# Optimization experiments

Measured on AMD Instinct MI355X. Metric: run time of the kernel, lower is better.

## Reference

```python
import jax, jax.numpy as jnp
import numpy as np

R, N, IN_F, OUT_F = 8, 4096, 64, 64


def setup_inputs() -> dict:
    key = jax.random.key(0)
    k_adj, k_x, k_w = jax.random.split(key, 3)
    adjacency = jax.random.uniform(k_adj, (R, N, N), dtype=jnp.float32)
    x = jax.random.normal(k_x, (N, IN_F), dtype=jnp.float32)
    weight = jax.random.uniform(k_w, (R, OUT_F, IN_F), dtype=jnp.float32)
    return {"adjacency": adjacency, "x": x, "weight": weight}


def reference(adjacency, x, weight):
    # y = sum_r (A[r] @ x) @ W[r].T
    # messages: [R, N, IN_F]
    msgs = jnp.einsum("rnm,mi->rni", adjacency, x)
    # transform per relation and sum over relations: [N, OUT_F]
    y = jnp.einsum("rni,roi->no", msgs, weight)
    return y
```

## Files before the change

kernel.cpp:

```cpp
#include <hip/hip_runtime.h>
#include <hip/hip_bf16.h>

#define RR 8
#define NN 4096
#define FF 64

typedef float f32x4 __attribute__((ext_vector_type(4)));
typedef short bf16x8 __attribute__((ext_vector_type(8)));

__device__ __forceinline__ short f2b(float f) {
  __hip_bfloat16 h = __float2bfloat16(f);
  return __builtin_bit_cast(short, h);
}

__device__ __forceinline__ bf16x8 cvt8(f32x4 lo, f32x4 hi) {
  bf16x8 r;
  r[0] = f2b(lo[0]); r[1] = f2b(lo[1]); r[2] = f2b(lo[2]); r[3] = f2b(lo[3]);
  r[4] = f2b(hi[0]); r[5] = f2b(hi[1]); r[6] = f2b(hi[2]); r[7] = f2b(hi[3]);
  return r;
}

__global__ __launch_bounds__(256) void compute_zt(const float* __restrict__ x,
                                                  const float* __restrict__ w,
                                                  short* __restrict__ zt) {
  const int tid   = threadIdx.x;
  const int lane  = tid & 63;
  const int wv    = tid >> 6;
  const int row16 = lane & 15;
  const int quad  = lane >> 4;
  const int r     = blockIdx.y;
  const int m0    = blockIdx.x * 64 + wv * 16;

  bf16x8 bfr[2];
#pragma unroll
  for (int s = 0; s < 2; ++s) {
    const float* p = x + (size_t)(m0 + row16) * FF + s * 32 + quad * 8;
    bfr[s] = cvt8(*(const f32x4*)p, *(const f32x4*)(p + 4));
  }

  f32x4 acc[4] = {{0.f,0.f,0.f,0.f},{0.f,0.f,0.f,0.f},
                  {0.f,0.f,0.f,0.f},{0.f,0.f,0.f,0.f}};
#pragma unroll
  for (int og = 0; og < 4; ++og) {
#pragma unroll
    for (int s = 0; s < 2; ++s) {
      const float* p = w + ((size_t)r * FF + og * 16 + row16) * FF + s * 32 + quad * 8;
      bf16x8 afr = cvt8(*(const f32x4*)p, *(const f32x4*)(p + 4));
      acc[og] = __builtin_amdgcn_mfma_f32_16x16x32_bf16(afr, bfr[s], acc[og], 0, 0, 0);
    }
  }

#pragma unroll
  for (int og = 0; og < 4; ++og)
#pragma unroll
    for (int j = 0; j < 4; ++j) {
      int o = og * 16 + quad * 4 + j;
      int m = m0 + row16;
      zt[((size_t)r * FF + o) * NN + m] = f2b(acc[og][j]);
    }
}


#define BK    128
#define NSTG  16
#define LROW  136

__device__ __forceinline__ void issueA(const float* __restrict__ abase,
                                       int trow, int tcol, int s, f32x4* av) {
#pragma unroll
  for (int i = 0; i < 8; ++i)
    av[i] = *(const f32x4*)(abase + (size_t)(i * 8 + trow) * NN + s * BK + tcol);
}

__device__ __forceinline__ void writeA(short* __restrict__ buf,
                                       int trow, int tcol, const f32x4* av) {
#pragma unroll
  for (int i = 0; i < 8; ++i) {
    short4 wv4;
    wv4.x = f2b(av[i][0]); wv4.y = f2b(av[i][1]);
    wv4.z = f2b(av[i][2]); wv4.w = f2b(av[i][3]);
    *(short4*)(buf + (i * 8 + trow) * LROW + tcol) = wv4;
  }
}

__device__ __forceinline__ void loadB4(const short* __restrict__ zb, int k, bf16x8* b) {
#pragma unroll
  for (int cg = 0; cg < 4; ++cg)
    b[cg] = *(const bf16x8*)(zb + (size_t)cg * 16 * NN + k);
}

__device__ __forceinline__ void mfma4(bf16x8 a, const bf16x8* b, f32x4* acc) {
  acc[0] = __builtin_amdgcn_mfma_f32_16x16x32_bf16(a, b[0], acc[0], 0, 0, 0);
  acc[1] = __builtin_amdgcn_mfma_f32_16x16x32_bf16(a, b[1], acc[1], 0, 0, 0);
  acc[2] = __builtin_amdgcn_mfma_f32_16x16x32_bf16(a, b[2], acc[2], 0, 0, 0);
  acc[3] = __builtin_amdgcn_mfma_f32_16x16x32_bf16(a, b[3], acc[3], 0, 0, 0);
}

__global__ __launch_bounds__(256, 3) void rgcn_main(const float* __restrict__ adj,
                                                    const short* __restrict__ zt,
                                                    float* __restrict__ partial) {
  __shared__ short lds[2][64 * LROW];

  const int tid   = threadIdx.x;
  const int lane  = tid & 63;
  const int wv    = tid >> 6;
  const int row16 = lane & 15;
  const int quad  = lane >> 4;

  const int nt   = blockIdx.x;
  const int rk   = blockIdx.y;
  const int r    = rk >> 1;
  const int half = rk & 1;
  const int n0   = nt * 64;

  const int trow = tid >> 5;
  const int tcol = (tid & 31) * 4;

  const float* abase = adj + (size_t)r * NN * NN + (size_t)n0 * NN + half * 2048;
  const short* zb    = zt + (size_t)r * FF * NN + (size_t)row16 * NN
                          + half * 2048 + quad * 8;

  f32x4 acc[4] = {{0.f,0.f,0.f,0.f},{0.f,0.f,0.f,0.f},
                  {0.f,0.f,0.f,0.f},{0.f,0.f,0.f,0.f}};
  f32x4 av[8];

  issueA(abase, trow, tcol, 0, av);
  writeA(&lds[0][0], trow, tcol, av);
  issueA(abase, trow, tcol, 1, av);
  __syncthreads();

#pragma unroll 1
  for (int s = 0; s < NSTG; ++s) {
    const short* fb = &lds[s & 1][(wv * 16 + row16) * LROW + quad * 8];

    bf16x8 b0[4], b1[4];
    loadB4(zb, s * BK,      b0);
    loadB4(zb, s * BK + 32, b1);

    bf16x8 a0 = *(const bf16x8*)(fb + 0);
    mfma4(a0, b0, acc);
    loadB4(zb, s * BK + 64, b0);
    bf16x8 a1 = *(const bf16x8*)(fb + 32);
    mfma4(a1, b1, acc);
    loadB4(zb, s * BK + 96, b1);
    bf16x8 a2 = *(const bf16x8*)(fb + 64);
    mfma4(a2, b0, acc);
    bf16x8 a3 = *(const bf16x8*)(fb + 96);
    mfma4(a3, b1, acc);

    if (s < NSTG - 1) {
      writeA(&lds[(s + 1) & 1][0], trow, tcol, av);
      if (s < NSTG - 2) issueA(abase, trow, tcol, s + 2, av);
      __syncthreads();
    }
  }

  float* pb = partial + ((size_t)rk * NN + n0) * FF;
#pragma unroll
  for (int cg = 0; cg < 4; ++cg)
#pragma unroll
    for (int j = 0; j < 4; ++j)
      pb[(size_t)(wv * 16 + quad * 4 + j) * FF + cg * 16 + row16] = acc[cg][j];
}

__global__ __launch_bounds__(256) void reduce_partials(const f32x4* __restrict__ p,
                                                       f32x4* __restrict__ out) {
  const int idx = blockIdx.x * 256 + threadIdx.x;
  f32x4 s = {0.f, 0.f, 0.f, 0.f};
#pragma unroll
  for (int rk = 0; rk < 16; ++rk)
    s += p[(size_t)rk * (NN * FF / 4) + idx];
  out[idx] = s;
}

extern "C" void kernel_launch(void* const* d_in, const int* in_sizes, int n_in,
                              void* d_out, int out_size, void* d_ws, size_t ws_size,
                              hipStream_t stream) {
  const float* adj = (const float*)d_in[0];
  const float* x   = (const float*)d_in[1];
  const float* w   = (const float*)d_in[2];
  float* out = (float*)d_out;

  short* zt      = (short*)d_ws;
  float* partial = (float*)((char*)d_ws + (16u << 20));

  compute_zt<<<dim3(NN / 64, RR), 256, 0, stream>>>(x, w, zt);
  rgcn_main<<<dim3(NN / 64, RR * 2), 256, 0, stream>>>(adj, zt, partial);
  reduce_partials<<<dim3(NN * FF / 4 / 256), 256, 0, stream>>>(
      (const f32x4*)partial, (f32x4*)out);
}
```

Baseline: 733.3 us.

## Drop LDS staging: per-wave register double-buffered direct loads with 4-way K split

```diff
diff --git a/kernel.cpp b/kernel.cpp
--- a/kernel.cpp
+++ b/kernel.cpp
@@ -60,107 +60,89 @@
     }
 }
 
+#define QK  1024
+#define NCH (QK / 32)
 
-#define BK    128
-#define NSTG  16
-#define LROW  136
+struct FragSet {
+  f32x4  aAlo, aAhi, aBlo, aBhi;
+  bf16x8 b0, b1, b2, b3;
+};
 
-__device__ __forceinline__ void issueA(const float* __restrict__ abase,
-                                       int trow, int tcol, int s, f32x4* av) {
-#pragma unroll
-  for (int i = 0; i < 8; ++i)
-    av[i] = *(const f32x4*)(abase + (size_t)(i * 8 + trow) * NN + s * BK + tcol);
+__device__ __forceinline__ void loadF(FragSet& F, const float* __restrict__ aA,
+                                      const float* __restrict__ aB,
+                                      const short* __restrict__ zb, int c) {
+  const float* pa = aA + c * 32;
+  F.aAlo = *(const f32x4*)pa;
+  F.aAhi = *(const f32x4*)(pa + 4);
+  const float* pb = aB + c * 32;
+  F.aBlo = *(const f32x4*)pb;
+  F.aBhi = *(const f32x4*)(pb + 4);
+  const short* pz = zb + c * 32;
+  F.b0 = *(const bf16x8*)pz;
+  F.b1 = *(const bf16x8*)(pz + 16 * NN);
+  F.b2 = *(const bf16x8*)(pz + 32 * NN);
+  F.b3 = *(const bf16x8*)(pz + 48 * NN);
 }
 
-__device__ __forceinline__ void writeA(short* __restrict__ buf,
-                                       int trow, int tcol, const f32x4* av) {
-#pragma unroll
-  for (int i = 0; i < 8; ++i) {
-    short4 wv4;
-    wv4.x = f2b(av[i][0]); wv4.y = f2b(av[i][1]);
-    wv4.z = f2b(av[i][2]); wv4.w = f2b(av[i][3]);
-    *(short4*)(buf + (i * 8 + trow) * LROW + tcol) = wv4;
-  }
+__device__ __forceinline__ void compF(const FragSet& F, f32x4* acc) {
+  bf16x8 afA = cvt8(F.aAlo, F.aAhi);
+  bf16x8 afB = cvt8(F.aBlo, F.aBhi);
+  acc[0] = __builtin_amdgcn_mfma_f32_16x16x32_bf16(afA, F.b0, acc[0], 0, 0, 0);
+  acc[1] = __builtin_amdgcn_mfma_f32_16x16x32_bf16(afA, F.b1, acc[1], 0, 0, 0);
+  acc[2] = __builtin_amdgcn_mfma_f32_16x16x32_bf16(afA, F.b2, acc[2], 0, 0, 0);
+  acc[3] = __builtin_amdgcn_mfma_f32_16x16x32_bf16(afA, F.b3, acc[3], 0, 0, 0);
+  acc[4] = __builtin_amdgcn_mfma_f32_16x16x32_bf16(afB, F.b0, acc[4], 0, 0, 0);
+  acc[5] = __builtin_amdgcn_mfma_f32_16x16x32_bf16(afB, F.b1, acc[5], 0, 0, 0);
+  acc[6] = __builtin_amdgcn_mfma_f32_16x16x32_bf16(afB, F.b2, acc[6], 0, 0, 0);
+  acc[7] = __builtin_amdgcn_mfma_f32_16x16x32_bf16(afB, F.b3, acc[7], 0, 0, 0);
 }
 
-__device__ __forceinline__ void loadB4(const short* __restrict__ zb, int k, bf16x8* b) {
-#pragma unroll
-  for (int cg = 0; cg < 4; ++cg)
-    b[cg] = *(const bf16x8*)(zb + (size_t)cg * 16 * NN + k);
-}
-
-__device__ __forceinline__ void mfma4(bf16x8 a, const bf16x8* b, f32x4* acc) {
-  acc[0] = __builtin_amdgcn_mfma_f32_16x16x32_bf16(a, b[0], acc[0], 0, 0, 0);
-  acc[1] = __builtin_amdgcn_mfma_f32_16x16x32_bf16(a, b[1], acc[1], 0, 0, 0);
-  acc[2] = __builtin_amdgcn_mfma_f32_16x16x32_bf16(a, b[2], acc[2], 0, 0, 0);
-  acc[3] = __builtin_amdgcn_mfma_f32_16x16x32_bf16(a, b[3], acc[3], 0, 0, 0);
-}
-
-__global__ __launch_bounds__(256, 3) void rgcn_main(const float* __restrict__ adj,
+__global__ __launch_bounds__(256, 4) void rgcn_main(const float* __restrict__ adj,
                                                     const short* __restrict__ zt,
                                                     float* __restrict__ partial) {
-  __shared__ short lds[2][64 * LROW];
-
   const int tid   = threadIdx.x;
   const int lane  = tid & 63;
   const int wv    = tid >> 6;
   const int row16 = lane & 15;
   const int quad  = lane >> 4;
 
-  const int nt   = blockIdx.x;
-  const int rk   = blockIdx.y;
-  const int r    = rk >> 1;
-  const int half = rk & 1;
-  const int n0   = nt * 64;
+  const int bid     = blockIdx.x;
+  const int r       = bid & 7;
+  const int u       = (bid >> 3) * 4 + wv;
+  const int q       = u >> 7;
+  const int rowtile = u & 127;
+  const int n0      = rowtile * 32;
+  const int k0      = q * QK;
 
-  const int trow = tid >> 5;
-  const int tcol = (tid & 31) * 4;
+  const float* aA = adj + ((size_t)r * NN + n0 + row16) * NN + k0 + quad * 8;
+  const float* aB = aA + (size_t)16 * NN;
+  const short* zb = zt + ((size_t)r * FF + row16) * NN + k0 + quad * 8;
 
-  const float* abase = adj + (size_t)r * NN * NN + (size_t)n0 * NN + half * 2048;
-  const short* zb    = zt + (size_t)r * FF * NN + (size_t)row16 * NN
-                          + half * 2048 + quad * 8;
+  f32x4 acc[8] = {{0.f,0.f,0.f,0.f},{0.f,0.f,0.f,0.f},{0.f,0.f,0.f,0.f},
+                  {0.f,0.f,0.f,0.f},{0.f,0.f,0.f,0.f},{0.f,0.f,0.f,0.f},
+                  {0.f,0.f,0.f,0.f},{0.f,0.f,0.f,0.f}};
 
-  f32x4 acc[4] = {{0.f,0.f,0.f,0.f},{0.f,0.f,0.f,0.f},
-                  {0.f,0.f,0.f,0.f},{0.f,0.f,0.f,0.f}};
-  f32x4 av[8];
+  FragSet F0, F1;
+  loadF(F0, aA, aB, zb, 0);
+#pragma unroll 1
+  for (int it = 0; it < NCH / 2 - 1; ++it) {
+    loadF(F1, aA, aB, zb, 2 * it + 1);
+    compF(F0, acc);
+    loadF(F0, aA, aB, zb, 2 * it + 2);
+    compF(F1, acc);
+  }
+  loadF(F1, aA, aB, zb, NCH - 1);
+  compF(F0, acc);
+  compF(F1, acc);
 
-  issueA(abase, trow, tcol, 0, av);
-  writeA(&lds[0][0], trow, tcol, av);
-  issueA(abase, trow, tcol, 1, av);
-  __syncthreads();
-
-#pragma unroll 1
-  for (int s = 0; s < NSTG; ++s) {
-    const short* fb = &lds[s & 1][(wv * 16 + row16) * LROW + quad * 8];
-
-    bf16x8 b0[4], b1[4];
-    loadB4(zb, s * BK,      b0);
-    loadB4(zb, s * BK + 32, b1);
-
-    bf16x8 a0 = *(const bf16x8*)(fb + 0);
-    mfma4(a0, b0, acc);
-    loadB4(zb, s * BK + 64, b0);
-    bf16x8 a1 = *(const bf16x8*)(fb + 32);
-    mfma4(a1, b1, acc);
-    loadB4(zb, s * BK + 96, b1);
-    bf16x8 a2 = *(const bf16x8*)(fb + 64);
-    mfma4(a2, b0, acc);
-    bf16x8 a3 = *(const bf16x8*)(fb + 96);
-    mfma4(a3, b1, acc);
-
-    if (s < NSTG - 1) {
-      writeA(&lds[(s + 1) & 1][0], trow, tcol, av);
-      if (s < NSTG - 2) issueA(abase, trow, tcol, s + 2, av);
-      __syncthreads();
-    }
-  }
-
-  float* pb = partial + ((size_t)rk * NN + n0) * FF;
+  float* pb = partial + ((size_t)(r * 4 + q) * NN + n0) * FF;
 #pragma unroll
-  for (int cg = 0; cg < 4; ++cg)
+  for (int g = 0; g < 2; ++g)
 #pragma unroll
-    for (int j = 0; j < 4; ++j)
-      pb[(size_t)(wv * 16 + quad * 4 + j) * FF + cg * 16 + row16] = acc[cg][j];
+    for (int cg = 0; cg < 4; ++cg)
+#pragma unroll
+      for (int j = 0; j < 4; ++j)
+        pb[(size_t)(g * 16 + quad * 4 + j) * FF + cg * 16 + row16] = acc[g * 4 + cg][j];
 }
 
 __global__ __launch_bounds__(256) void reduce_partials(const f32x4* __restrict__ p,
@@ -168,8 +150,8 @@
   const int idx = blockIdx.x * 256 + threadIdx.x;
   f32x4 s = {0.f, 0.f, 0.f, 0.f};
 #pragma unroll
-  for (int rk = 0; rk < 16; ++rk)
-    s += p[(size_t)rk * (NN * FF / 4) + idx];
+  for (int sl = 0; sl < 32; ++sl)
+    s += p[(size_t)sl * (NN * FF / 4) + idx];
   out[idx] = s;
 }
 
@@ -185,7 +167,7 @@
   float* partial = (float*)((char*)d_ws + (16u << 20));
 
   compute_zt<<<dim3(NN / 64, RR), 256, 0, stream>>>(x, w, zt);
-  rgcn_main<<<dim3(NN / 64, RR * 2), 256, 0, stream>>>(adj, zt, partial);
+  rgcn_main<<<dim3(1024), 256, 0, stream>>>(adj, zt, partial);
   reduce_partials<<<dim3(NN * FF / 4 / 256), 256, 0, stream>>>(
       (const f32x4*)partial, (f32x4*)out);
 }
```

Measured after the change: 751.1 us. +2.4%, slower.
